# Kernel tuning notes

Hardware: AMD Instinct MI355X
Metric: run time of the kernel (lower is better)

The kernel has to match this reference:

```python
import jax, jax.numpy as jnp
import numpy as np

D_MODEL = 1024
NUM_HEADS = 16
D_HEAD = D_MODEL // NUM_HEADS
BATCH, SEQ, MEM = 2, 1024, 1024
TOT = SEQ + MEM


def setup_inputs() -> dict:
    key = jax.random.key(0)
    ks = jax.random.split(key, 16)
    s = 0.02
    return {
        "x": jax.random.normal(ks[0], (BATCH, SEQ, D_MODEL), jnp.float32),
        "mem": jax.random.normal(ks[1], (BATCH, MEM, D_MODEL), jnp.float32),
        "mask": jnp.zeros((1, 1, SEQ, TOT), jnp.float32),
        "rel_enc": jax.random.normal(ks[2], (TOT, D_MODEL), jnp.float32),
        "Wq": jax.random.normal(ks[3], (D_MODEL, D_MODEL), jnp.float32) * s,
        "bq": jnp.zeros((D_MODEL,), jnp.float32),
        "Wke": jax.random.normal(ks[4], (D_MODEL, D_MODEL), jnp.float32) * s,
        "bke": jnp.zeros((D_MODEL,), jnp.float32),
        "Wkr": jax.random.normal(ks[5], (D_MODEL, D_MODEL), jnp.float32) * s,
        "bkr": jnp.zeros((D_MODEL,), jnp.float32),
        "Wv": jax.random.normal(ks[6], (D_MODEL, D_MODEL), jnp.float32) * s,
        "bv": jnp.zeros((D_MODEL,), jnp.float32),
        "Wo": jax.random.normal(ks[7], (D_MODEL, D_MODEL), jnp.float32) * s,
        "bo": jnp.zeros((D_MODEL,), jnp.float32),
    }


def _split_heads(t, b):
    # (b, s, d_model) -> (b, h, s, d_head)
    return t.reshape(b, -1, NUM_HEADS, D_HEAD).transpose(0, 2, 1, 3)


def _rel_enc_shift(arr):
    # arr: (b, h, l, m) -> Transformer-XL shift trick
    b, h, l, m = arr.shape
    arr = jnp.concatenate([arr, jnp.zeros((b, h, l, 1), arr.dtype)], axis=-1)
    arr = arr.reshape(b, h, l * (m + 1))
    return arr[:, :, l - 1:-1].reshape(b, h, l, m)


def reference(x, mem, mask, rel_enc, Wq, bq, Wke, bke, Wkr, bkr, Wv, bv, Wo, bo):
    b, s, _ = x.shape
    x_tilde = jnp.concatenate([mem, x], axis=1)  # (b, tot, d)
    q = _split_heads(x @ Wq + bq, b)             # (b, h, s, dh)
    k = _split_heads(x_tilde @ Wke + bke, b)     # (b, h, tot, dh)
    v = _split_heads(x_tilde @ Wv + bv, b)       # (b, h, tot, dh)
    A = jnp.einsum("bhsd,bhtd->bhst", q, k)      # content scores
    Q = (rel_enc @ Wkr + bkr).reshape(-1, NUM_HEADS, D_HEAD).transpose(1, 0, 2)  # (h, tot, dh)
    B_hat = jnp.einsum("bhsd,htd->bhst", q, Q)
    B = _rel_enc_shift(B_hat)                    # relative-position scores
    scores = (A + B) / jnp.sqrt(jnp.float32(D_HEAD)) + mask * -1e9
    w = jax.nn.softmax(scores, axis=-1)
    out = jnp.einsum("bhst,bhtd->bhsd", w, v)
    out = out.transpose(0, 2, 1, 3).reshape(b, s, D_MODEL)
    return out @ Wo + bo
```

## Files before the change

### kernel.cpp

```cpp
#include <hip/hip_runtime.h>

typedef unsigned short ushort;
typedef unsigned int uint;
typedef __attribute__((ext_vector_type(8))) short short8;
typedef __attribute__((ext_vector_type(4))) float float4v;

#define D_MODEL 1024
#define NH 16
#define DH 64
#define BATCH 2
#define SEQ 1024
#define MEMLEN 1024
#define TOT 2048

__device__ __forceinline__ float b2f(ushort u) {
  return __uint_as_float(((uint)u) << 16);
}
__device__ __forceinline__ ushort f2b(float f) {
  uint i = __float_as_uint(f);
  uint r = (i + 0x7fffu + ((i >> 16) & 1u)) >> 16;
  return (ushort)r;
}
__device__ __forceinline__ void gld16(const ushort* g, ushort* l) {
  __builtin_amdgcn_global_load_lds(
      (const __attribute__((address_space(1))) void*)g,
      (__attribute__((address_space(3))) void*)l, 16, 0, 0);
}

__global__ __launch_bounds__(256) void preproc_kernel(
    const float* __restrict__ x, const float* __restrict__ mem,
    const float* __restrict__ rel, const float* __restrict__ mask,
    ushort* __restrict__ xt, ushort* __restrict__ xb,
    ushort* __restrict__ relb, ushort* __restrict__ maskb) {
  const int bid = blockIdx.x;
  if (bid < 2048) {
    int idx = bid * 256 + threadIdx.x;
    int row = idx >> 7;
    int c8 = (idx & 127) << 3;
    int b = row >> 11;
    int i = row & 2047;
    const float* src = (i < MEMLEN) ? &mem[((b << 10) + i) * D_MODEL]
                                    : &x[((b << 10) + (i - MEMLEN)) * D_MODEL];
    float4 f0 = *(const float4*)(&src[c8]);
    float4 f1 = *(const float4*)(&src[c8 + 4]);
    ushort u[8] = {f2b(f0.x), f2b(f0.y), f2b(f0.z), f2b(f0.w),
                   f2b(f1.x), f2b(f1.y), f2b(f1.z), f2b(f1.w)};
    *(uint4*)(&xt[row * D_MODEL + c8]) = *(const uint4*)u;
    if (i >= MEMLEN)
      *(uint4*)(&xb[((b << 10) + (i - MEMLEN)) * D_MODEL + c8]) =
          *(const uint4*)u;
  } else if (bid < 3072) {
    int idx = (bid - 2048) * 256 + threadIdx.x;
    int base = idx << 3;
    float4 f0 = *(const float4*)(&rel[base]);
    float4 f1 = *(const float4*)(&rel[base + 4]);
    ushort u[8] = {f2b(f0.x), f2b(f0.y), f2b(f0.z), f2b(f0.w),
                   f2b(f1.x), f2b(f1.y), f2b(f1.z), f2b(f1.w)};
    *(uint4*)(&relb[base]) = *(const uint4*)u;
  } else {
    int idx = (bid - 3072) * 256 + threadIdx.x;
    int base = idx << 3;
    float4 f0 = *(const float4*)(&mask[base]);
    float4 f1 = *(const float4*)(&mask[base + 4]);
    ushort u[8] = {f2b(f0.x * -1e9f), f2b(f0.y * -1e9f), f2b(f0.z * -1e9f),
                   f2b(f0.w * -1e9f), f2b(f1.x * -1e9f), f2b(f1.y * -1e9f),
                   f2b(f1.z * -1e9f), f2b(f1.w * -1e9f)};
    *(uint4*)(&maskb[base]) = *(const uint4*)u;
  }
}

__global__ __launch_bounds__(256) void transpose_cvt5_kernel(
    const float* __restrict__ W0, const float* __restrict__ W1,
    const float* __restrict__ W2, const float* __restrict__ W3,
    const float* __restrict__ W4, ushort* __restrict__ T0,
    ushort* __restrict__ T1, ushort* __restrict__ T2, ushort* __restrict__ T3,
    ushort* __restrict__ T4) {
  __shared__ ushort tle[32][33];
  const float* W;
  ushort* T;
  switch (blockIdx.z) {
    case 0: W = W0; T = T0; break;
    case 1: W = W1; T = T1; break;
    case 2: W = W2; T = T2; break;
    case 3: W = W3; T = T3; break;
    default: W = W4; T = T4; break;
  }
  const int bx = blockIdx.x * 32, by = blockIdx.y * 32;
  const int tx = threadIdx.x & 31, ty = threadIdx.x >> 5;
#pragma unroll
  for (int j = 0; j < 32; j += 8)
    tle[ty + j][tx] = f2b(W[(by + ty + j) * 1024 + bx + tx]);
  __syncthreads();
#pragma unroll
  for (int j = 0; j < 32; j += 8)
    T[(bx + ty + j) * 1024 + by + tx] = tle[tx][ty + j];
}

__global__ __launch_bounds__(256) void gemm_fused_kernel(
    const ushort* __restrict__ xt, const ushort* __restrict__ xbrel,
    const ushort* __restrict__ WkeT, const ushort* __restrict__ WqT,
    const ushort* __restrict__ WkrT, const float* __restrict__ bke,
    const float* __restrict__ bv, const float* __restrict__ bq,
    const float* __restrict__ bkr, ushort* __restrict__ kv,
    ushort* __restrict__ qr) {
  __shared__ ushort As[128 * 32];
  __shared__ ushort Bs[128 * 32];
  const int bid = blockIdx.x;
  const bool seg0 = (bid < 512);
  const ushort* A;
  const ushort* BT;
  int m0, n0;
  if (seg0) {
    m0 = (bid & 31) * 128;
    n0 = (bid >> 5) * 128;
    A = xt;
    BT = WkeT;
  } else {
    int g = bid - 512;
    m0 = (g & 31) * 128;
    n0 = (g >> 5) * 128;
    A = xbrel;
    BT = (m0 < 2048) ? WqT : WkrT;
  }
  const int tid = threadIdx.x;
  const int w = tid >> 6, lane = tid & 63, m15 = lane & 15, q4 = lane >> 4;
  const int wm = w & 1, wn = w >> 1;
  float4v acc[4][4] = {};
  const int c0 = tid, c1 = tid + 256;
  const int r0 = c0 >> 2, u0 = (c0 & 3) * 8;
  const int r1 = c1 >> 2, u1 = (c1 & 3) * 8;

  for (int kk = 0; kk < 1024; kk += 32) {
    __syncthreads();
    gld16(&A[(m0 + r0) * 1024 + kk + u0], &As[c0 * 8]);
    gld16(&A[(m0 + r1) * 1024 + kk + u1], &As[c1 * 8]);
    gld16(&BT[(n0 + r0) * 1024 + kk + u0], &Bs[c0 * 8]);
    gld16(&BT[(n0 + r1) * 1024 + kk + u1], &Bs[c1 * 8]);
    __syncthreads();
    short8 af[4], bf[4];
#pragma unroll
    for (int i = 0; i < 4; ++i)
      af[i] = *(const short8*)(&As[(wm * 64 + i * 16 + m15) * 32 + q4 * 8]);
#pragma unroll
    for (int j = 0; j < 4; ++j)
      bf[j] = *(const short8*)(&Bs[(wn * 64 + j * 16 + m15) * 32 + q4 * 8]);
#pragma unroll
    for (int i = 0; i < 4; ++i)
#pragma unroll
      for (int j = 0; j < 4; ++j)
        acc[i][j] =
            __builtin_amdgcn_mfma_f32_16x16x32_bf16(af[i], bf[j], acc[i][j], 0, 0, 0);
  }
#pragma unroll
  for (int j = 0; j < 4; ++j) {
    int col = n0 + wn * 64 + j * 16 + m15;
    if (seg0) {
      if (col < 1024) {
        float bb = bke[col];
#pragma unroll
        for (int i = 0; i < 4; ++i) {
          int rowb = m0 + wm * 64 + i * 16 + q4 * 4;
#pragma unroll
          for (int r = 0; r < 4; ++r)
            kv[(rowb + r) * 2048 + col] = f2b((acc[i][j][r] + bb) * 0.125f);
        }
      } else {
        float bb = bv[col - 1024];
#pragma unroll
        for (int i = 0; i < 4; ++i) {
          int rowb = m0 + wm * 64 + i * 16 + q4 * 4;
          int dg = ((rowb >> 11) << 10) + (col - 1024);
          size_t prow = (size_t)(dg * 2 + ((rowb >> 10) & 1)) * 2048 + 1024 +
                        (rowb & 1023);
          uint lo = (uint)f2b(acc[i][j][0] + bb) |
                    ((uint)f2b(acc[i][j][1] + bb) << 16);
          uint hi = (uint)f2b(acc[i][j][2] + bb) |
                    ((uint)f2b(acc[i][j][3] + bb) << 16);
          *(uint2*)(&kv[prow]) = make_uint2(lo, hi);
        }
      }
    } else {
      float bb = (m0 < 2048) ? bq[col] : bkr[col];
      float sc = (m0 < 2048) ? 1.0f : 0.125f;
#pragma unroll
      for (int i = 0; i < 4; ++i) {
        int rowb = m0 + wm * 64 + i * 16 + q4 * 4;
#pragma unroll
        for (int r = 0; r < 4; ++r)
          qr[(rowb + r) * 1024 + col] = f2b((acc[i][j][r] + bb) * sc);
      }
    }
  }
}

template <int EPI>
__global__ __launch_bounds__(256) void gemm64_kernel(
    const ushort* __restrict__ A, const ushort* __restrict__ BT,
    const float* __restrict__ bias, void* __restrict__ Cout, int M, int N,
    int K) {
  __shared__ ushort As[64 * 32];
  __shared__ ushort Bs[128 * 32];
  const int m0 = blockIdx.x * 64, n0 = blockIdx.y * 128;
  const int tid = threadIdx.x;
  const int w = tid >> 6, lane = tid & 63, m15 = lane & 15, q4 = lane >> 4;
  float4v acc[4][2] = {};
  const int ra = tid >> 2, ua = (tid & 3) * 8;
  const int c0 = tid, c1 = tid + 256;
  const int rb0 = c0 >> 2, ub0 = (c0 & 3) * 8;
  const int rb1 = c1 >> 2, ub1 = (c1 & 3) * 8;

  for (int kk = 0; kk < K; kk += 32) {
    __syncthreads();
    gld16(&A[(m0 + ra) * K + kk + ua], &As[tid * 8]);
    gld16(&BT[(n0 + rb0) * K + kk + ub0], &Bs[c0 * 8]);
    gld16(&BT[(n0 + rb1) * K + kk + ub1], &Bs[c1 * 8]);
    __syncthreads();
    short8 bf[2];
#pragma unroll
    for (int j = 0; j < 2; ++j)
      bf[j] = *(const short8*)(&Bs[(w * 32 + j * 16 + m15) * 32 + q4 * 8]);
#pragma unroll
    for (int i = 0; i < 4; ++i) {
      short8 af = *(const short8*)(&As[(i * 16 + m15) * 32 + q4 * 8]);
#pragma unroll
      for (int j = 0; j < 2; ++j)
        acc[i][j] =
            __builtin_amdgcn_mfma_f32_16x16x32_bf16(af, bf[j], acc[i][j], 0, 0, 0);
    }
  }
#pragma unroll
  for (int j = 0; j < 2; ++j) {
    int col = n0 + w * 32 + j * 16 + m15;
    float bv = bias[col];
#pragma unroll
    for (int i = 0; i < 4; ++i) {
      int rowb = m0 + i * 16 + q4 * 4;
#pragma unroll
      for (int r = 0; r < 4; ++r) {
        float v = acc[i][j][r] + bv;
        if (EPI == 1)
          ((float*)Cout)[(rowb + r) * N + col] = v;
        else
          ((ushort*)Cout)[(rowb + r) * N + col] = f2b(v);
      }
    }
  }
}

__global__ __launch_bounds__(256) void bhat_kernel(
    const ushort* __restrict__ q, const ushort* __restrict__ Qrb,
    const ushort* __restrict__ maskb, ushort* __restrict__ Bh) {
  __shared__ ushort As[2 * 128 * 32];
  __shared__ ushort Bs[2 * 128 * 32];
  const int bs0 = blockIdx.x * 128, u0 = blockIdx.y * 128, h = blockIdx.z;
  const int tid = threadIdx.x;
  const int w = tid >> 6, lane = tid & 63, m15 = lane & 15, q4 = lane >> 4;
  const int wm = w & 1, wn = w >> 1;

#pragma unroll
  for (int c = 0; c < 4; ++c) {
    int unit = c * 256 + tid;
    int row = (unit >> 2) & 127, kh = unit >> 9, cu = unit & 3;
    gld16(&q[(bs0 + row) * 1024 + (h << 6) + kh * 32 + cu * 8], &As[unit * 8]);
    gld16(&Qrb[(u0 + row) * 1024 + (h << 6) + kh * 32 + cu * 8], &Bs[unit * 8]);
  }
  __syncthreads();

  float4v acc[4][4] = {};
#pragma unroll
  for (int kh = 0; kh < 2; ++kh) {
    short8 af[4], bf[4];
#pragma unroll
    for (int i = 0; i < 4; ++i)
      af[i] = *(const short8*)(&As[kh * 4096 + (wm * 64 + i * 16 + m15) * 32 + q4 * 8]);
#pragma unroll
    for (int j = 0; j < 4; ++j)
      bf[j] = *(const short8*)(&Bs[kh * 4096 + (wn * 64 + j * 16 + m15) * 32 + q4 * 8]);
#pragma unroll
    for (int i = 0; i < 4; ++i)
#pragma unroll
      for (int j = 0; j < 4; ++j)
        acc[i][j] =
            __builtin_amdgcn_mfma_f32_16x16x32_bf16(af[i], bf[j], acc[i][j], 0, 0, 0);
  }
  const int b = bs0 >> 10;
  const int s0loc = bs0 & 1023;
  const int outrow0 = ((b << 4) + h) * 1024 + s0loc;
#pragma unroll
  for (int j = 0; j < 4; ++j) {
    int u = u0 + wn * 64 + j * 16 + m15;
#pragma unroll
    for (int i = 0; i < 4; ++i) {
      int rowb = outrow0 + wm * 64 + i * 16 + q4 * 4;
      int spb = s0loc + wm * 64 + i * 16 + q4 * 4;
#pragma unroll
      for (int r = 0; r < 4; ++r) {
        int sp = spb + r;
        bool selA = (u >= 1023 - sp);
        int mrow = selA ? sp : (sp > 0 ? sp - 1 : 0);
        int mcol = selA ? (u + sp - 1023) : (u + sp + 1025);
        float mval = b2f(maskb[mrow * 2048 + mcol]);
        Bh[(rowb + r) * 2048 + u] = f2b(acc[i][j][r] + mval);
      }
    }
  }
}

__global__ __launch_bounds__(256) void attn_kernel(
    const ushort* __restrict__ qb, const ushort* __restrict__ kv,
    const ushort* __restrict__ Bh, const ushort* __restrict__ maskb,
    ushort* __restrict__ attn) {
  __shared__ ushort Pp[4][16 * 36];
  __shared__ float comb[2][16][68];
  __shared__ float csum[32];

  const int tid = threadIdx.x;
  const int w = tid >> 6, lane = tid & 63, m15 = lane & 15, q4 = lane >> 4;
  const int st = w & 1, th = w >> 1;
  const int s0w = blockIdx.x * 32 + st * 16;
  const int h = blockIdx.y, b = blockIdx.z;
  const int s_l = q4 * 4;

  const ushort* qp = &qb[((b << 10) + s0w + m15) * 1024 + (h << 6) + q4 * 8];
  const short8 af0 = *(const short8*)qp;
  const short8 af1 = *(const short8*)(qp + 32);

  const ushort* kvb = &kv[((size_t)(b << 11) * 2048) + (h << 6)];
  const ushort* vrowb =
      &kv[((size_t)(((b << 10) + (h << 6)) << 1) + th) * 2048 + 1024];
  const int bhbase = ((b << 4) + h) << 21;
  ushort* pw = &Pp[w][0];

  int offA[4], offB[4], diagT[4];
  float dm[4];
#pragma unroll
  for (int i = 0; i < 4; ++i) {
    int s = s0w + s_l + i;
    offA[i] = bhbase + (s << 11) - s + 1023;
    offB[i] = bhbase + ((s + 1) << 11) - s - 1026;
    diagT[i] = s + 1025;
    dm[i] = (diagT[i] <= 2047) ? b2f(maskb[s * 2048 + diagT[i]]) : 0.f;
  }

  float lsum4[4] = {0.f, 0.f, 0.f, 0.f};
  float4v oacc[4] = {};

  auto pre_bh = [&](int t0, uint (&B)[4]) {
#pragma unroll
    for (int nt = 0; nt < 2; ++nt)
#pragma unroll
      for (int ip = 0; ip < 2; ++ip) {
        uint pk = 0;
#pragma unroll
        for (int k = 0; k < 2; ++k) {
          int i = ip * 2 + k;
          int t = t0 + nt * 16 + m15;
          int off = (t < diagT[i]) ? offA[i] : offB[i];
          ushort v = Bh[off + t];
          pk |= ((uint)v) << (16 * k);
        }
        B[nt * 2 + ip] = pk;
      }
  };

  auto loadKV = [&](int t0, short8 (&Kr)[2][2], short8 (&Vr)[4]) {
#pragma unroll
    for (int nt = 0; nt < 2; ++nt) {
      const ushort* kp = &kvb[(size_t)(t0 + nt * 16 + m15) * 2048 + q4 * 8];
      Kr[nt][0] = *(const short8*)kp;
      Kr[nt][1] = *(const short8*)(kp + 32);
    }
    int tc = (t0 & 1023) + q4 * 8;
#pragma unroll
    for (int nd = 0; nd < 4; ++nd)
      Vr[nd] = *(const short8*)(&vrowb[(size_t)(nd * 16 + m15) * 4096 + tc]);
  };

  auto work = [&](int t0, short8 (&Kr)[2][2], short8 (&Vr)[4], uint (&B)[4]) {
    float4v a0 = {}, a1 = {};
    a0 = __builtin_amdgcn_mfma_f32_16x16x32_bf16(af0, Kr[0][0], a0, 0, 0, 0);
    a0 = __builtin_amdgcn_mfma_f32_16x16x32_bf16(af1, Kr[0][1], a0, 0, 0, 0);
    a1 = __builtin_amdgcn_mfma_f32_16x16x32_bf16(af0, Kr[1][0], a1, 0, 0, 0);
    a1 = __builtin_amdgcn_mfma_f32_16x16x32_bf16(af1, Kr[1][1], a1, 0, 0, 0);
#pragma unroll
    for (int nt = 0; nt < 2; ++nt)
#pragma unroll
      for (int i = 0; i < 4; ++i) {
        int t = t0 + nt * 16 + m15;
        uint u = B[nt * 2 + (i >> 1)];
        uint bits = (i & 1) ? (u & 0xffff0000u) : (u << 16);
        float bv = (t == diagT[i]) ? dm[i] : __uint_as_float(bits);
        float a = (nt == 0) ? a0[i] : a1[i];
        float p = __expf(a + bv);
        lsum4[i] += p;
        pw[(s_l + i) * 36 + nt * 16 + m15] = f2b(p);
      }
    short8 pfr = *(const short8*)(&pw[m15 * 36 + q4 * 8]);
#pragma unroll
    for (int nd = 0; nd < 4; ++nd)
      oacc[nd] =
          __builtin_amdgcn_mfma_f32_16x16x32_bf16(pfr, Vr[nd], oacc[nd], 0, 0, 0);
  };

  const int tb = th * 1024;
  uint Bb0[4], Bb1[4], Bn0[4], Bn1[4];
  pre_bh(tb, Bb0);
  pre_bh(tb + 32, Bb1);
  pre_bh(tb + 64, Bn0);
  pre_bh(tb + 96, Bn1);
  for (int p = 0; p < 16; ++p) {
    const int t0 = tb + p * 64;
    short8 K0[2][2], V0[4], K1[2][2], V1[4];
    loadKV(t0, K0, V0);
    loadKV(t0 + 32, K1, V1);
    __builtin_amdgcn_sched_barrier(0);
    uint Bt0[4], Bt1[4];
    if (p < 14) {
      pre_bh(t0 + 128, Bt0);
      pre_bh(t0 + 160, Bt1);
    }
    __builtin_amdgcn_sched_barrier(0);
    work(t0, K0, V0, Bb0);
    work(t0 + 32, K1, V1, Bb1);
#pragma unroll
    for (int j = 0; j < 4; ++j) {
      Bb0[j] = Bn0[j];
      Bb1[j] = Bn1[j];
    }
    if (p < 14) {
#pragma unroll
      for (int j = 0; j < 4; ++j) {
        Bn0[j] = Bt0[j];
        Bn1[j] = Bt1[j];
      }
    }
  }

#pragma unroll
  for (int i = 0; i < 4; ++i) {
    float v = lsum4[i];
    v += __shfl_xor(v, 1, 64);
    v += __shfl_xor(v, 2, 64);
    v += __shfl_xor(v, 4, 64);
    v += __shfl_xor(v, 8, 64);
    lsum4[i] = v;
  }
  if (th == 1) {
#pragma unroll
    for (int nd = 0; nd < 4; ++nd)
#pragma unroll
      for (int i = 0; i < 4; ++i)
        comb[st][s_l + i][nd * 16 + m15] = oacc[nd][i];
    if (m15 == 0)
#pragma unroll
      for (int i = 0; i < 4; ++i) csum[st * 16 + s_l + i] = lsum4[i];
  }
  __syncthreads();
  if (th == 0) {
#pragma unroll
    for (int i = 0; i < 4; ++i) lsum4[i] += csum[st * 16 + s_l + i];
#pragma unroll
    for (int nd = 0; nd < 4; ++nd)
#pragma unroll
      for (int i = 0; i < 4; ++i) {
        float v = oacc[nd][i] + comb[st][s_l + i][nd * 16 + m15];
        attn[((b << 10) + s0w + s_l + i) * 1024 + (h << 6) + nd * 16 + m15] =
            f2b(v / lsum4[i]);
      }
  }
}

extern "C" void kernel_launch(void* const* d_in, const int* in_sizes, int n_in,
                              void* d_out, int out_size, void* d_ws,
                              size_t ws_size, hipStream_t stream) {
  const float* x = (const float*)d_in[0];
  const float* mem = (const float*)d_in[1];
  const float* mask = (const float*)d_in[2];
  const float* rel = (const float*)d_in[3];
  const float* Wq = (const float*)d_in[4];
  const float* bq = (const float*)d_in[5];
  const float* Wke = (const float*)d_in[6];
  const float* bke = (const float*)d_in[7];
  const float* Wkr = (const float*)d_in[8];
  const float* bkr = (const float*)d_in[9];
  const float* Wv = (const float*)d_in[10];
  const float* bv = (const float*)d_in[11];
  const float* Wo = (const float*)d_in[12];
  const float* bo = (const float*)d_in[13];
  float* out = (float*)d_out;

  ushort* ws = (ushort*)d_ws;
  ushort* xt = ws;
  ushort* xbrel = xt + 4096 * 1024;
  ushort* WqT = xbrel + 4096 * 1024;
  ushort* WkeT = WqT + 1024 * 1024;
  ushort* WvT = WkeT + 1024 * 1024;
  ushort* WkrT = WvT + 1024 * 1024;
  ushort* WoT = WkrT + 1024 * 1024;
  ushort* kv = WoT + 1024 * 1024;
  ushort* qr = kv + 4096 * 2048;
  ushort* attn = qr + 4096 * 1024;
  ushort* maskb = attn + 2048 * 1024;
  ushort* Bh = maskb + 1024 * 2048;
  ushort* relb = xbrel + 2048 * 1024;
  ushort* Qrb = qr + 2048 * 1024;

  preproc_kernel<<<4096, 256, 0, stream>>>(x, mem, rel, mask, xt, xbrel, relb,
                                           maskb);
  transpose_cvt5_kernel<<<dim3(32, 32, 5), 256, 0, stream>>>(
      Wq, Wke, Wkr, Wv, Wo, WqT, WkeT, WkrT, WvT, WoT);

  gemm_fused_kernel<<<768, 256, 0, stream>>>(xt, xbrel, WkeT, WqT, WkrT, bke,
                                             bv, bq, bkr, kv, qr);

  bhat_kernel<<<dim3(16, 16, 16), 256, 0, stream>>>(qr, Qrb, maskb, Bh);

  attn_kernel<<<dim3(SEQ / 32, NH, BATCH), 256, 0, stream>>>(qr, kv, Bh, maskb,
                                                             attn);

  gemm64_kernel<1><<<dim3(32, 8), 256, 0, stream>>>(attn, WoT, bo, out, 2048,
                                                    1024, 1024);
}
```

Baseline: 372.4 us.

## Skew-pad B_hat rows for vector loads and stage bias and mask via LDS

The B_hat buffer is re-laid out with padded rows of 2056 elements and a per-row skew, so the Transformer-XL shifted diagonal reads in the attention kernel become aligned 16-byte vector loads instead of scalar gathers. Those vectors, plus the mask (now applied in the attention kernel rather than in bhat), are staged through per-wave LDS tiles. The main loop is restructured into 32-wide chunks with K prefetched one chunk ahead and B/mask a few chunks ahead. A scalar fallback path handles chunks near the shift boundary. The padded buffer is larger and needs enough workspace, and the boundary handling adds branch complexity.

```diff
diff --git a/kernel.cpp b/kernel.cpp
--- a/kernel.cpp
+++ b/kernel.cpp
@@ -12,6 +12,8 @@
 #define SEQ 1024
 #define MEMLEN 1024
 #define TOT 2048
+#define BROW 2056
+#define PLN (1024 * BROW)
 
 __device__ __forceinline__ float b2f(ushort u) {
   return __uint_as_float(((uint)u) << 16);
@@ -249,7 +251,7 @@
 
 __global__ __launch_bounds__(256) void bhat_kernel(
     const ushort* __restrict__ q, const ushort* __restrict__ Qrb,
-    const ushort* __restrict__ maskb, ushort* __restrict__ Bh) {
+    ushort* __restrict__ Bh) {
   __shared__ ushort As[2 * 128 * 32];
   __shared__ ushort Bs[2 * 128 * 32];
   const int bs0 = blockIdx.x * 128, u0 = blockIdx.y * 128, h = blockIdx.z;
@@ -285,22 +287,17 @@
   }
   const int b = bs0 >> 10;
   const int s0loc = bs0 & 1023;
-  const int outrow0 = ((b << 4) + h) * 1024 + s0loc;
+  const int pbase = ((b << 4) + h) * PLN;
 #pragma unroll
   for (int j = 0; j < 4; ++j) {
     int u = u0 + wn * 64 + j * 16 + m15;
 #pragma unroll
     for (int i = 0; i < 4; ++i) {
-      int rowb = outrow0 + wm * 64 + i * 16 + q4 * 4;
       int spb = s0loc + wm * 64 + i * 16 + q4 * 4;
 #pragma unroll
       for (int r = 0; r < 4; ++r) {
         int sp = spb + r;
-        bool selA = (u >= 1023 - sp);
-        int mrow = selA ? sp : (sp > 0 ? sp - 1 : 0);
-        int mcol = selA ? (u + sp - 1023) : (u + sp + 1025);
-        float mval = b2f(maskb[mrow * 2048 + mcol]);
-        Bh[(rowb + r) * 2048 + u] = f2b(acc[i][j][r] + mval);
+        Bh[pbase + sp * BROW + ((sp + 1) & 7) + u] = f2b(acc[i][j][r]);
       }
     }
   }
@@ -310,6 +307,8 @@
     const ushort* __restrict__ qb, const ushort* __restrict__ kv,
     const ushort* __restrict__ Bh, const ushort* __restrict__ maskb,
     ushort* __restrict__ attn) {
+  __shared__ ushort Bt[4][512];
+  __shared__ ushort Mt[4][512];
   __shared__ ushort Pp[4][16 * 36];
   __shared__ float comb[2][16][68];
   __shared__ float csum[32];
@@ -328,112 +327,114 @@
   const ushort* kvb = &kv[((size_t)(b << 11) * 2048) + (h << 6)];
   const ushort* vrowb =
       &kv[((size_t)(((b << 10) + (h << 6)) << 1) + th) * 2048 + 1024];
-  const int bhbase = ((b << 4) + h) << 21;
+  const int bhbase = ((b << 4) + h) * PLN;
   ushort* pw = &Pp[w][0];
+  ushort* btw = &Bt[w][0];
+  ushort* mtw = &Mt[w][0];
+
+  const int lr = lane >> 2, lc = (lane & 3) * 8;
+  const int sA = s0w + lr;
+  const int vOffA = bhbase + sA * BROW + ((sA + 1) & 7) - sA + 1023;
+  const int vOffB = bhbase + (sA + 1) * BROW + ((sA + 2) & 7) - sA - 1026;
+  const int vDiag = sA + 1025;
+  const ushort* mrow = &maskb[sA * 2048];
 
   int offA[4], offB[4], diagT[4];
-  float dm[4];
 #pragma unroll
   for (int i = 0; i < 4; ++i) {
     int s = s0w + s_l + i;
-    offA[i] = bhbase + (s << 11) - s + 1023;
-    offB[i] = bhbase + ((s + 1) << 11) - s - 1026;
+    offA[i] = bhbase + s * BROW + ((s + 1) & 7) - s + 1023;
+    offB[i] = bhbase + (s + 1) * BROW + ((s + 2) & 7) - s - 1026;
     diagT[i] = s + 1025;
-    dm[i] = (diagT[i] <= 2047) ? b2f(maskb[s * 2048 + diagT[i]]) : 0.f;
   }
 
   float lsum4[4] = {0.f, 0.f, 0.f, 0.f};
   float4v oacc[4] = {};
-
-  auto pre_bh = [&](int t0, uint (&B)[4]) {
-#pragma unroll
-    for (int nt = 0; nt < 2; ++nt)
-#pragma unroll
-      for (int ip = 0; ip < 2; ++ip) {
-        uint pk = 0;
-#pragma unroll
-        for (int k = 0; k < 2; ++k) {
-          int i = ip * 2 + k;
-          int t = t0 + nt * 16 + m15;
-          int off = (t < diagT[i]) ? offA[i] : offB[i];
-          ushort v = Bh[off + t];
-          pk |= ((uint)v) << (16 * k);
-        }
-        B[nt * 2 + ip] = pk;
-      }
+  const int tb = th * 1024;
+
+  auto vB = [&](int c) -> short8 {
+    int t = tb + c * 32 + lc;
+    int off = (t + 7 < vDiag) ? vOffA : vOffB;
+    return *(const short8*)(&Bh[off + t]);
   };
-
-  auto loadKV = [&](int t0, short8 (&Kr)[2][2], short8 (&Vr)[4]) {
+  auto vM = [&](int c) -> short8 {
+    return *(const short8*)(&mrow[tb + c * 32 + lc]);
+  };
+  auto ldK = [&](int c, short8 (&K)[2][2]) {
+    int t0 = tb + c * 32;
 #pragma unroll
     for (int nt = 0; nt < 2; ++nt) {
       const ushort* kp = &kvb[(size_t)(t0 + nt * 16 + m15) * 2048 + q4 * 8];
-      Kr[nt][0] = *(const short8*)kp;
-      Kr[nt][1] = *(const short8*)(kp + 32);
-    }
-    int tc = (t0 & 1023) + q4 * 8;
-#pragma unroll
-    for (int nd = 0; nd < 4; ++nd)
-      Vr[nd] = *(const short8*)(&vrowb[(size_t)(nd * 16 + m15) * 4096 + tc]);
+      K[nt][0] = *(const short8*)kp;
+      K[nt][1] = *(const short8*)(kp + 32);
+    }
   };
 
-  auto work = [&](int t0, short8 (&Kr)[2][2], short8 (&Vr)[4], uint (&B)[4]) {
+  auto chunk = [&](int c, short8& Bc, short8& Mc, short8 (&Kc)[2][2],
+                   short8 (&Kn)[2][2]) {
+    const int t0 = tb + c * 32;
+    *(short8*)(&btw[lane * 8]) = Bc;
+    *(short8*)(&mtw[lane * 8]) = Mc;
+    short8 Vc[4];
+    {
+      int tc = c * 32 + q4 * 8;
+#pragma unroll
+      for (int nd = 0; nd < 4; ++nd)
+        Vc[nd] = *(const short8*)(&vrowb[(size_t)(nd * 16 + m15) * 4096 + tc]);
+    }
+    if (c < 31) ldK(c + 1, Kn);
+    Bc = vB(c + 4 <= 31 ? c + 4 : 31);
+    Mc = vM(c + 2 <= 31 ? c + 2 : 31);
     float4v a0 = {}, a1 = {};
-    a0 = __builtin_amdgcn_mfma_f32_16x16x32_bf16(af0, Kr[0][0], a0, 0, 0, 0);
-    a0 = __builtin_amdgcn_mfma_f32_16x16x32_bf16(af1, Kr[0][1], a0, 0, 0, 0);
-    a1 = __builtin_amdgcn_mfma_f32_16x16x32_bf16(af0, Kr[1][0], a1, 0, 0, 0);
-    a1 = __builtin_amdgcn_mfma_f32_16x16x32_bf16(af1, Kr[1][1], a1, 0, 0, 0);
-#pragma unroll
-    for (int nt = 0; nt < 2; ++nt)
-#pragma unroll
-      for (int i = 0; i < 4; ++i) {
-        int t = t0 + nt * 16 + m15;
-        uint u = B[nt * 2 + (i >> 1)];
-        uint bits = (i & 1) ? (u & 0xffff0000u) : (u << 16);
-        float bv = (t == diagT[i]) ? dm[i] : __uint_as_float(bits);
-        float a = (nt == 0) ? a0[i] : a1[i];
-        float p = __expf(a + bv);
-        lsum4[i] += p;
-        pw[(s_l + i) * 36 + nt * 16 + m15] = f2b(p);
-      }
+    a0 = __builtin_amdgcn_mfma_f32_16x16x32_bf16(af0, Kc[0][0], a0, 0, 0, 0);
+    a0 = __builtin_amdgcn_mfma_f32_16x16x32_bf16(af1, Kc[0][1], a0, 0, 0, 0);
+    a1 = __builtin_amdgcn_mfma_f32_16x16x32_bf16(af0, Kc[1][0], a1, 0, 0, 0);
+    a1 = __builtin_amdgcn_mfma_f32_16x16x32_bf16(af1, Kc[1][1], a1, 0, 0, 0);
+    const bool slow = (t0 + 31 >= s0w + 1025) && (t0 <= s0w + 1040);
+    if (!slow) {
+#pragma unroll
+      for (int nt = 0; nt < 2; ++nt)
+#pragma unroll
+        for (int i = 0; i < 4; ++i) {
+          int li = (s_l + i) * 32 + nt * 16 + m15;
+          float a = (nt == 0) ? a0[i] : a1[i];
+          float p = __expf(a + b2f(btw[li]) + b2f(mtw[li]));
+          lsum4[i] += p;
+          pw[(s_l + i) * 36 + nt * 16 + m15] = f2b(p);
+        }
+    } else {
+#pragma unroll
+      for (int nt = 0; nt < 2; ++nt)
+#pragma unroll
+        for (int i = 0; i < 4; ++i) {
+          int t = t0 + nt * 16 + m15;
+          int li = (s_l + i) * 32 + nt * 16 + m15;
+          float bv = (t == diagT[i])
+                         ? 0.f
+                         : b2f(Bh[((t < diagT[i]) ? offA[i] : offB[i]) + t]);
+          float a = (nt == 0) ? a0[i] : a1[i];
+          float p = __expf(a + bv + b2f(mtw[li]));
+          lsum4[i] += p;
+          pw[(s_l + i) * 36 + nt * 16 + m15] = f2b(p);
+        }
+    }
     short8 pfr = *(const short8*)(&pw[m15 * 36 + q4 * 8]);
 #pragma unroll
     for (int nd = 0; nd < 4; ++nd)
       oacc[nd] =
-          __builtin_amdgcn_mfma_f32_16x16x32_bf16(pfr, Vr[nd], oacc[nd], 0, 0, 0);
+          __builtin_amdgcn_mfma_f32_16x16x32_bf16(pfr, Vc[nd], oacc[nd], 0, 0, 0);
   };
 
-  const int tb = th * 1024;
-  uint Bb0[4], Bb1[4], Bn0[4], Bn1[4];
-  pre_bh(tb, Bb0);
-  pre_bh(tb + 32, Bb1);
-  pre_bh(tb + 64, Bn0);
-  pre_bh(tb + 96, Bn1);
-  for (int p = 0; p < 16; ++p) {
-    const int t0 = tb + p * 64;
-    short8 K0[2][2], V0[4], K1[2][2], V1[4];
-    loadKV(t0, K0, V0);
-    loadKV(t0 + 32, K1, V1);
-    __builtin_amdgcn_sched_barrier(0);
-    uint Bt0[4], Bt1[4];
-    if (p < 14) {
-      pre_bh(t0 + 128, Bt0);
-      pre_bh(t0 + 160, Bt1);
-    }
-    __builtin_amdgcn_sched_barrier(0);
-    work(t0, K0, V0, Bb0);
-    work(t0 + 32, K1, V1, Bb1);
-#pragma unroll
-    for (int j = 0; j < 4; ++j) {
-      Bb0[j] = Bn0[j];
-      Bb1[j] = Bn1[j];
-    }
-    if (p < 14) {
-#pragma unroll
-      for (int j = 0; j < 4; ++j) {
-        Bn0[j] = Bt0[j];
-        Bn1[j] = Bt1[j];
-      }
-    }
+  short8 B0 = vB(0), B1 = vB(1), B2 = vB(2), B3 = vB(3);
+  short8 M0 = vM(0), M1 = vM(1);
+  short8 Ka[2][2], Kb[2][2];
+  ldK(0, Ka);
+  for (int j = 0; j < 8; ++j) {
+    int c = j * 4;
+    chunk(c, B0, M0, Ka, Kb);
+    chunk(c + 1, B1, M1, Kb, Ka);
+    chunk(c + 2, B2, M0, Ka, Kb);
+    chunk(c + 3, B3, M1, Kb, Ka);
   }
 
 #pragma unroll
@@ -513,7 +514,7 @@
   gemm_fused_kernel<<<768, 256, 0, stream>>>(xt, xbrel, WkeT, WqT, WkrT, bke,
                                              bv, bq, bkr, kv, qr);
 
-  bhat_kernel<<<dim3(16, 16, 16), 256, 0, stream>>>(qr, Qrb, maskb, Bh);
+  bhat_kernel<<<dim3(16, 16, 16), 256, 0, stream>>>(qr, Qrb, Bh);
 
   attn_kernel<<<dim3(SEQ / 32, NH, BATCH), 256, 0, stream>>>(qr, kv, Bh, maskb,
                                                              attn);
```

Result: faster. 364.3 us (-2.2%).

## Software-pipeline K/V loads two chunks ahead and Bh loads four chunks ahead in attention

Applied to the files above, without the earlier changes.

Restructures the attention inner loop into a rotating four-buffer software pipeline. The K/V fragments for chunk c+2 and the relative-position scores for chunk c+4 are loaded while chunk c is computed, replacing the old pattern that loaded K/V at the start of each 64-wide step and waited on them. The scores are now stored as unpacked ushorts. The sched_barrier masks allow partial reordering, and launch_bounds(256,2) caps registers to allow two blocks per CU. The extra buffers raise register pressure, and the new register cap could cause spills.

```diff
diff --git a/kernel.cpp b/kernel.cpp
--- a/kernel.cpp
+++ b/kernel.cpp
@@ -306,7 +306,7 @@
   }
 }
 
-__global__ __launch_bounds__(256) void attn_kernel(
+__global__ __launch_bounds__(256, 2) void attn_kernel(
     const ushort* __restrict__ qb, const ushort* __restrict__ kv,
     const ushort* __restrict__ Bh, const ushort* __restrict__ maskb,
     ushort* __restrict__ attn) {
@@ -344,52 +344,54 @@
 
   float lsum4[4] = {0.f, 0.f, 0.f, 0.f};
   float4v oacc[4] = {};
-
-  auto pre_bh = [&](int t0, uint (&B)[4]) {
-#pragma unroll
-    for (int nt = 0; nt < 2; ++nt)
-#pragma unroll
-      for (int ip = 0; ip < 2; ++ip) {
-        uint pk = 0;
-#pragma unroll
-        for (int k = 0; k < 2; ++k) {
-          int i = ip * 2 + k;
-          int t = t0 + nt * 16 + m15;
-          int off = (t < diagT[i]) ? offA[i] : offB[i];
-          ushort v = Bh[off + t];
-          pk |= ((uint)v) << (16 * k);
-        }
-        B[nt * 2 + ip] = pk;
-      }
-  };
-
-  auto loadKV = [&](int t0, short8 (&Kr)[2][2], short8 (&Vr)[4]) {
+  const int tb = th * 1024;
+
+  auto ldKV = [&](int c, short8 (&K)[2][2], short8 (&V)[4]) {
+    const int t0 = tb + c * 32;
 #pragma unroll
     for (int nt = 0; nt < 2; ++nt) {
       const ushort* kp = &kvb[(size_t)(t0 + nt * 16 + m15) * 2048 + q4 * 8];
-      Kr[nt][0] = *(const short8*)kp;
-      Kr[nt][1] = *(const short8*)(kp + 32);
+      K[nt][0] = *(const short8*)kp;
+      K[nt][1] = *(const short8*)(kp + 32);
     }
-    int tc = (t0 & 1023) + q4 * 8;
+    const int tc = c * 32 + q4 * 8;
 #pragma unroll
     for (int nd = 0; nd < 4; ++nd)
-      Vr[nd] = *(const short8*)(&vrowb[(size_t)(nd * 16 + m15) * 4096 + tc]);
+      V[nd] = *(const short8*)(&vrowb[(size_t)(nd * 16 + m15) * 4096 + tc]);
   };
-
-  auto work = [&](int t0, short8 (&Kr)[2][2], short8 (&Vr)[4], uint (&B)[4]) {
-    float4v a0 = {}, a1 = {};
-    a0 = __builtin_amdgcn_mfma_f32_16x16x32_bf16(af0, Kr[0][0], a0, 0, 0, 0);
-    a0 = __builtin_amdgcn_mfma_f32_16x16x32_bf16(af1, Kr[0][1], a0, 0, 0, 0);
-    a1 = __builtin_amdgcn_mfma_f32_16x16x32_bf16(af0, Kr[1][0], a1, 0, 0, 0);
-    a1 = __builtin_amdgcn_mfma_f32_16x16x32_bf16(af1, Kr[1][1], a1, 0, 0, 0);
+  auto ldB = [&](int c, ushort (&B)[8]) {
+    const int t0 = tb + c * 32;
 #pragma unroll
     for (int nt = 0; nt < 2; ++nt)
 #pragma unroll
       for (int i = 0; i < 4; ++i) {
         int t = t0 + nt * 16 + m15;
-        uint u = B[nt * 2 + (i >> 1)];
-        uint bits = (i & 1) ? (u & 0xffff0000u) : (u << 16);
-        float bv = (t == diagT[i]) ? dm[i] : __uint_as_float(bits);
+        int off = (t < diagT[i]) ? offA[i] : offB[i];
+        B[nt * 4 + i] = Bh[off + t];
+      }
+  };
+
+  auto chunk = [&](int c, short8 (&K)[2][2], short8 (&V)[4],
+                   short8 (&Kp)[2][2], short8 (&Vp)[4], ushort (&Bs)[8]) {
+    ushort cur[8];
+#pragma unroll
+    for (int j = 0; j < 8; ++j) cur[j] = Bs[j];
+    if (c + 2 < 32) ldKV(c + 2, Kp, Vp);
+    __builtin_amdgcn_sched_barrier(0x38F);
+    if (c + 4 < 32) ldB(c + 4, Bs);
+    __builtin_amdgcn_sched_barrier(0x38F);
+    float4v a0 = {}, a1 = {};
+    a0 = __builtin_amdgcn_mfma_f32_16x16x32_bf16(af0, K[0][0], a0, 0, 0, 0);
+    a0 = __builtin_amdgcn_mfma_f32_16x16x32_bf16(af1, K[0][1], a0, 0, 0, 0);
+    a1 = __builtin_amdgcn_mfma_f32_16x16x32_bf16(af0, K[1][0], a1, 0, 0, 0);
+    a1 = __builtin_amdgcn_mfma_f32_16x16x32_bf16(af1, K[1][1], a1, 0, 0, 0);
+    const int t0 = tb + c * 32;
+#pragma unroll
+    for (int nt = 0; nt < 2; ++nt)
+#pragma unroll
+      for (int i = 0; i < 4; ++i) {
+        int t = t0 + nt * 16 + m15;
+        float bv = (t == diagT[i]) ? dm[i] : b2f(cur[nt * 4 + i]);
         float a = (nt == 0) ? a0[i] : a1[i];
         float p = __expf(a + bv);
         lsum4[i] += p;
@@ -399,41 +401,25 @@
 #pragma unroll
     for (int nd = 0; nd < 4; ++nd)
       oacc[nd] =
-          __builtin_amdgcn_mfma_f32_16x16x32_bf16(pfr, Vr[nd], oacc[nd], 0, 0, 0);
+          __builtin_amdgcn_mfma_f32_16x16x32_bf16(pfr, V[nd], oacc[nd], 0, 0, 0);
   };
 
-  const int tb = th * 1024;
-  uint Bb0[4], Bb1[4], Bn0[4], Bn1[4];
-  pre_bh(tb, Bb0);
-  pre_bh(tb + 32, Bb1);
-  pre_bh(tb + 64, Bn0);
-  pre_bh(tb + 96, Bn1);
-  for (int p = 0; p < 16; ++p) {
-    const int t0 = tb + p * 64;
-    short8 K0[2][2], V0[4], K1[2][2], V1[4];
-    loadKV(t0, K0, V0);
-    loadKV(t0 + 32, K1, V1);
-    __builtin_amdgcn_sched_barrier(0);
-    uint Bt0[4], Bt1[4];
-    if (p < 14) {
-      pre_bh(t0 + 128, Bt0);
-      pre_bh(t0 + 160, Bt1);
-    }
-    __builtin_amdgcn_sched_barrier(0);
-    work(t0, K0, V0, Bb0);
-    work(t0 + 32, K1, V1, Bb1);
-#pragma unroll
-    for (int j = 0; j < 4; ++j) {
-      Bb0[j] = Bn0[j];
-      Bb1[j] = Bn1[j];
-    }
-    if (p < 14) {
-#pragma unroll
-      for (int j = 0; j < 4; ++j) {
-        Bn0[j] = Bt0[j];
-        Bn1[j] = Bt1[j];
-      }
-    }
+  short8 K0[2][2], V0[4], K1[2][2], V1[4], K2[2][2], V2[4], K3[2][2], V3[4];
+  ushort B0[8], B1[8], B2[8], B3[8];
+  ldKV(0, K0, V0);
+  ldKV(1, K1, V1);
+  __builtin_amdgcn_sched_barrier(0x38F);
+  ldB(0, B0);
+  ldB(1, B1);
+  ldB(2, B2);
+  ldB(3, B3);
+  __builtin_amdgcn_sched_barrier(0x38F);
+  for (int j = 0; j < 8; ++j) {
+    const int c = j * 4;
+    chunk(c, K0, V0, K2, V2, B0);
+    chunk(c + 1, K1, V1, K3, V3, B1);
+    chunk(c + 2, K2, V2, K0, V0, B2);
+    chunk(c + 3, K3, V3, K1, V1, B3);
   }
 
 #pragma unroll
```

Result: no change. 366.4 us (-1.6%).
